# Optimization experiments

Measured on AMD Instinct MI355X. Metric: run time of the kernel, lower is better.

The kernel has to match this reference:

```python
import jax, jax.numpy as jnp
import numpy as np

B, N, DEG = 256, 16384, 32  # batch, num_neurons, fan-in per neuron

def setup_inputs() -> dict:
    key = jax.random.key(0)
    kx, kw, ki = jax.random.split(key, 3)
    x = jax.random.normal(kx, (B, N), dtype=jnp.float32)
    w = jax.random.normal(kw, (N, DEG), dtype=jnp.float32)  # nonzero weights per neuron
    idx = jax.random.randint(ki, (N, DEG), 0, N)            # source-neuron indices per neuron
    return {"x": x, "w": w, "idx": idx}

def reference(x, w, idx):
    # Per neuron j: gather its fan-in channels and apply Dense(1) with
    # kernel = nonzero weights, then relu; concat over neurons == axis N.
    gathered = x[:, idx]                      # [B, N, DEG] gather
    out = jnp.einsum('bnd,nd->bn', gathered, w)  # sparse matvec per batch row
    return jax.nn.relu(out)                   # [B, N]
```

## Files before the change

### kernel.cpp

```cpp
#include <hip/hip_runtime.h>


#define NB   16384
#define DEG  32

typedef __fp16 hp2 __attribute__((ext_vector_type(2)));

__device__ __forceinline__ unsigned pk16(float a, float b) {
    return __builtin_bit_cast(unsigned, (hp2)__builtin_amdgcn_cvt_pkrtz(a, b));
}

__global__ __launch_bounds__(256) void prep_pw_kernel(
    const int* __restrict__ idx, const float* __restrict__ w,
    uint4* __restrict__ pw4) {
    __shared__ int   idx_s[64][33];
    __shared__ float w_s[64][33];
    const int t  = threadIdx.x;
    const int nb = (int)blockIdx.x * 64;

    const int4*   src  = (const int4*)(idx + (size_t)nb * DEG);
    const float4* srcw = (const float4*)(w   + (size_t)nb * DEG);
#pragma unroll
    for (int p = 0; p < 2; ++p) {
        const int e4 = t + 256 * p;
        const int n0 = e4 >> 3;
        const int c0 = (e4 & 7) * 4;
        const int4 v = src[e4];
        idx_s[n0][c0 + 0] = v.x; idx_s[n0][c0 + 1] = v.y;
        idx_s[n0][c0 + 2] = v.z; idx_s[n0][c0 + 3] = v.w;
        const float4 f = srcw[e4];
        w_s[n0][c0 + 0] = f.x; w_s[n0][c0 + 1] = f.y;
        w_s[n0][c0 + 2] = f.z; w_s[n0][c0 + 3] = f.w;
    }
    __syncthreads();

    const int np    = t & 63;
    const int dbase = t >> 6;
#pragma unroll
    for (int k = 0; k < 2; ++k) {
        const int d4 = dbase * 2 + k;
        const int c  = 4 * d4;
        uint4 o;
        o.x = (unsigned)idx_s[np][c + 0] | ((unsigned)idx_s[np][c + 1] << 16);
        o.y = pk16(w_s[np][c + 0], w_s[np][c + 1]);
        o.z = (unsigned)idx_s[np][c + 2] | ((unsigned)idx_s[np][c + 3] << 16);
        o.w = pk16(w_s[np][c + 2], w_s[np][c + 3]);
        pw4[(size_t)d4 * NB + nb + np] = o;
    }
}

#define LOADQ(buf, nn)                                                     \
    do {                                                                   \
        const uint4* p_ = pw4 + (nn);                                      \
        _Pragma("unroll") for (int d4_ = 0; d4_ < 8; ++d4_)                \
            buf[d4_] = p_[(size_t)d4_ * NB];                               \
    } while (0)

#define GISSUE(K)                                                          \
    {                                                                      \
        const unsigned jA_ = Q[K].x;                                       \
        g[K][0] = lds[jA_ & 0xffffu];                                      \
        g[K][1] = lds[jA_ >> 16];                                          \
        const unsigned jB_ = Q[K].z;                                       \
        g[K][2] = lds[jB_ & 0xffffu];                                      \
        g[K][3] = lds[jB_ >> 16];                                          \
    }

#define GFMA(K, r01, r23)                                                  \
    {                                                                      \
        const hp2 wA_  = __builtin_bit_cast(hp2, Q[K].y);                  \
        const hp2 wAlo = {wA_.x, wA_.x};                                   \
        const hp2 wAhi = {wA_.y, wA_.y};                                   \
        r01 += wAlo * __builtin_bit_cast(hp2, g[K][0].x);                  \
        r23 += wAlo * __builtin_bit_cast(hp2, g[K][0].y);                  \
        r01 += wAhi * __builtin_bit_cast(hp2, g[K][1].x);                  \
        r23 += wAhi * __builtin_bit_cast(hp2, g[K][1].y);                  \
        const hp2 wB_  = __builtin_bit_cast(hp2, Q[K].w);                  \
        const hp2 wBlo = {wB_.x, wB_.x};                                   \
        const hp2 wBhi = {wB_.y, wB_.y};                                   \
        r01 += wBlo * __builtin_bit_cast(hp2, g[K][2].x);                  \
        r23 += wBlo * __builtin_bit_cast(hp2, g[K][2].y);                  \
        r01 += wBhi * __builtin_bit_cast(hp2, g[K][3].x);                  \
        r23 += wBhi * __builtin_bit_cast(hp2, g[K][3].y);                  \
    }

#define STEP(I, LD)                                                        \
    {                                                                      \
        const int n = n0 + t + 1024 * (I);                                 \
        if (LD) LOADQ(Q, n);                                               \
        uint2 g[8][4];                                                     \
        GISSUE(0) GISSUE(1) GISSUE(2) GISSUE(3)                            \
        hp2 a01 = {0, 0}, a23 = {0, 0}, c01 = {0, 0}, c23 = {0, 0};        \
        GFMA(0, a01, a23) GISSUE(4)                                        \
        GFMA(1, a01, a23) GISSUE(5)                                        \
        GFMA(2, a01, a23) GISSUE(6)                                        \
        GFMA(3, a01, a23) GISSUE(7)                                        \
        GFMA(4, c01, c23)                                                  \
        GFMA(5, c01, c23)                                                  \
        GFMA(6, c01, c23)                                                  \
        GFMA(7, c01, c23)                                                  \
        const hp2 s01 = a01 + c01;                                         \
        const hp2 s23 = a23 + c23;                                         \
        __builtin_nontemporal_store(fmaxf((float)s01.x, 0.f),              \
                                    &out[(size_t)(b0 + 0) * NB + n]);      \
        __builtin_nontemporal_store(fmaxf((float)s01.y, 0.f),              \
                                    &out[(size_t)(b0 + 1) * NB + n]);      \
        __builtin_nontemporal_store(fmaxf((float)s23.x, 0.f),              \
                                    &out[(size_t)(b0 + 2) * NB + n]);      \
        __builtin_nontemporal_store(fmaxf((float)s23.y, 0.f),              \
                                    &out[(size_t)(b0 + 3) * NB + n]);      \
    }

__global__ __launch_bounds__(1024, 4) void gather4_kernel(
    const float* __restrict__ x, const uint4* __restrict__ pw4,
    float* __restrict__ out) {
    extern __shared__ uint2 lds[];
    const int t  = threadIdx.x;
    const int q  = (int)blockIdx.x & 63;
    const int n0 = ((int)blockIdx.x >> 6) * 4096;

    const float* xr0 = x + (size_t)(4 * q) * NB;
    const float* xr1 = xr0 + NB;
    const float* xr2 = xr1 + NB;
    const float* xr3 = xr2 + NB;
#pragma unroll
    for (int p = 0; p < 4; ++p) {
        const int j = 4 * (t + 1024 * p);
        const float4 r0 = *(const float4*)&xr0[j];
        const float4 r1 = *(const float4*)&xr1[j];
        const float4 r2 = *(const float4*)&xr2[j];
        const float4 r3 = *(const float4*)&xr3[j];
        uint4 w0, w1;
        w0.x = pk16(r0.x, r1.x); w0.y = pk16(r2.x, r3.x);
        w0.z = pk16(r0.y, r1.y); w0.w = pk16(r2.y, r3.y);
        w1.x = pk16(r0.z, r1.z); w1.y = pk16(r2.z, r3.z);
        w1.z = pk16(r0.w, r1.w); w1.w = pk16(r2.w, r3.w);
        *(uint4*)&lds[j]     = w0;
        *(uint4*)&lds[j + 2] = w1;
    }

    uint4 Q[8];
    LOADQ(Q, n0 + t);
    __syncthreads();

    const int b0 = 4 * q;
    STEP(0, 0)
    STEP(1, 1)
    STEP(2, 1)
    STEP(3, 1)
}

extern "C" void kernel_launch(void* const* d_in, const int* in_sizes, int n_in,
                              void* d_out, int out_size, void* d_ws, size_t ws_size,
                              hipStream_t stream) {
    const float* x   = (const float*)d_in[0];
    const float* w   = (const float*)d_in[1];
    const int*   idx = (const int*)d_in[2];
    float* out = (float*)d_out;
    uint4* pw4 = (uint4*)d_ws;

    (void)hipFuncSetAttribute((const void*)gather4_kernel,
                              hipFuncAttributeMaxDynamicSharedMemorySize, 131072);

    prep_pw_kernel<<<NB / 64, 256, 0, stream>>>(idx, w, pw4);

    gather4_kernel<<<256, 1024, 131072, stream>>>(x, pw4, out);
}
```

Before: 83.83 us.

## Process two batch rows per block instead of four to halve LDS footprint

```diff
diff --git a/kernel.cpp b/kernel.cpp
--- a/kernel.cpp
+++ b/kernel.cpp
@@ -59,91 +59,77 @@
 #define GISSUE(K)                                                          \
     {                                                                      \
         const unsigned jA_ = Q[K].x;                                       \
-        g[K][0] = lds[jA_ & 0xffffu];                                      \
-        g[K][1] = lds[jA_ >> 16];                                          \
+        g[K][0] = lds32[jA_ & 0xffffu];                                    \
+        g[K][1] = lds32[jA_ >> 16];                                        \
         const unsigned jB_ = Q[K].z;                                       \
-        g[K][2] = lds[jB_ & 0xffffu];                                      \
-        g[K][3] = lds[jB_ >> 16];                                          \
+        g[K][2] = lds32[jB_ & 0xffffu];                                    \
+        g[K][3] = lds32[jB_ >> 16];                                        \
     }
 
-#define GFMA(K, r01, r23)                                                  \
+#define GFMA(K, r01)                                                       \
     {                                                                      \
         const hp2 wA_  = __builtin_bit_cast(hp2, Q[K].y);                  \
         const hp2 wAlo = {wA_.x, wA_.x};                                   \
         const hp2 wAhi = {wA_.y, wA_.y};                                   \
-        r01 += wAlo * __builtin_bit_cast(hp2, g[K][0].x);                  \
-        r23 += wAlo * __builtin_bit_cast(hp2, g[K][0].y);                  \
-        r01 += wAhi * __builtin_bit_cast(hp2, g[K][1].x);                  \
-        r23 += wAhi * __builtin_bit_cast(hp2, g[K][1].y);                  \
+        r01 += wAlo * __builtin_bit_cast(hp2, g[K][0]);                    \
+        r01 += wAhi * __builtin_bit_cast(hp2, g[K][1]);                    \
         const hp2 wB_  = __builtin_bit_cast(hp2, Q[K].w);                  \
         const hp2 wBlo = {wB_.x, wB_.x};                                   \
         const hp2 wBhi = {wB_.y, wB_.y};                                   \
-        r01 += wBlo * __builtin_bit_cast(hp2, g[K][2].x);                  \
-        r23 += wBlo * __builtin_bit_cast(hp2, g[K][2].y);                  \
-        r01 += wBhi * __builtin_bit_cast(hp2, g[K][3].x);                  \
-        r23 += wBhi * __builtin_bit_cast(hp2, g[K][3].y);                  \
+        r01 += wBlo * __builtin_bit_cast(hp2, g[K][2]);                    \
+        r01 += wBhi * __builtin_bit_cast(hp2, g[K][3]);                    \
     }
 
 #define STEP(I, LD)                                                        \
     {                                                                      \
         const int n = n0 + t + 1024 * (I);                                 \
         if (LD) LOADQ(Q, n);                                               \
-        uint2 g[8][4];                                                     \
+        unsigned g[8][4];                                                  \
         GISSUE(0) GISSUE(1) GISSUE(2) GISSUE(3)                            \
-        hp2 a01 = {0, 0}, a23 = {0, 0}, c01 = {0, 0}, c23 = {0, 0};        \
-        GFMA(0, a01, a23) GISSUE(4)                                        \
-        GFMA(1, a01, a23) GISSUE(5)                                        \
-        GFMA(2, a01, a23) GISSUE(6)                                        \
-        GFMA(3, a01, a23) GISSUE(7)                                        \
-        GFMA(4, c01, c23)                                                  \
-        GFMA(5, c01, c23)                                                  \
-        GFMA(6, c01, c23)                                                  \
-        GFMA(7, c01, c23)                                                  \
+        hp2 a01 = {0, 0}, c01 = {0, 0};                                    \
+        GFMA(0, a01) GISSUE(4)                                             \
+        GFMA(1, a01) GISSUE(5)                                             \
+        GFMA(2, a01) GISSUE(6)                                             \
+        GFMA(3, a01) GISSUE(7)                                             \
+        GFMA(4, c01)                                                       \
+        GFMA(5, c01)                                                       \
+        GFMA(6, c01)                                                       \
+        GFMA(7, c01)                                                       \
         const hp2 s01 = a01 + c01;                                         \
-        const hp2 s23 = a23 + c23;                                         \
         __builtin_nontemporal_store(fmaxf((float)s01.x, 0.f),              \
                                     &out[(size_t)(b0 + 0) * NB + n]);      \
         __builtin_nontemporal_store(fmaxf((float)s01.y, 0.f),              \
                                     &out[(size_t)(b0 + 1) * NB + n]);      \
-        __builtin_nontemporal_store(fmaxf((float)s23.x, 0.f),              \
-                                    &out[(size_t)(b0 + 2) * NB + n]);      \
-        __builtin_nontemporal_store(fmaxf((float)s23.y, 0.f),              \
-                                    &out[(size_t)(b0 + 3) * NB + n]);      \
     }
 
-__global__ __launch_bounds__(1024, 4) void gather4_kernel(
+__global__ __launch_bounds__(1024, 8) void gather2_kernel(
     const float* __restrict__ x, const uint4* __restrict__ pw4,
     float* __restrict__ out) {
-    extern __shared__ uint2 lds[];
+    extern __shared__ unsigned lds32[];
     const int t  = threadIdx.x;
-    const int q  = (int)blockIdx.x & 63;
-    const int n0 = ((int)blockIdx.x >> 6) * 4096;
+    const int pr = (int)blockIdx.x & 127;
+    const int n0 = ((int)blockIdx.x >> 7) * 4096;
 
-    const float* xr0 = x + (size_t)(4 * q) * NB;
+    const float* xr0 = x + (size_t)(2 * pr) * NB;
     const float* xr1 = xr0 + NB;
-    const float* xr2 = xr1 + NB;
-    const float* xr3 = xr2 + NB;
 #pragma unroll
     for (int p = 0; p < 4; ++p) {
         const int j = 4 * (t + 1024 * p);
         const float4 r0 = *(const float4*)&xr0[j];
         const float4 r1 = *(const float4*)&xr1[j];
-        const float4 r2 = *(const float4*)&xr2[j];
-        const float4 r3 = *(const float4*)&xr3[j];
-        uint4 w0, w1;
-        w0.x = pk16(r0.x, r1.x); w0.y = pk16(r2.x, r3.x);
-        w0.z = pk16(r0.y, r1.y); w0.w = pk16(r2.y, r3.y);
-        w1.x = pk16(r0.z, r1.z); w1.y = pk16(r2.z, r3.z);
-        w1.z = pk16(r0.w, r1.w); w1.w = pk16(r2.w, r3.w);
-        *(uint4*)&lds[j]     = w0;
-        *(uint4*)&lds[j + 2] = w1;
+        uint4 w0;
+        w0.x = pk16(r0.x, r1.x);
+        w0.y = pk16(r0.y, r1.y);
+        w0.z = pk16(r0.z, r1.z);
+        w0.w = pk16(r0.w, r1.w);
+        *(uint4*)&lds32[j] = w0;
     }
 
     uint4 Q[8];
     LOADQ(Q, n0 + t);
     __syncthreads();
 
-    const int b0 = 4 * q;
+    const int b0 = 2 * pr;
     STEP(0, 0)
     STEP(1, 1)
     STEP(2, 1)
@@ -159,10 +145,10 @@
     float* out = (float*)d_out;
     uint4* pw4 = (uint4*)d_ws;
 
-    (void)hipFuncSetAttribute((const void*)gather4_kernel,
-                              hipFuncAttributeMaxDynamicSharedMemorySize, 131072);
+    (void)hipFuncSetAttribute((const void*)gather2_kernel,
+                              hipFuncAttributeMaxDynamicSharedMemorySize, 65536);
 
     prep_pw_kernel<<<NB / 64, 256, 0, stream>>>(idx, w, pw4);
 
-    gather4_kernel<<<256, 1024, 131072, stream>>>(x, pw4, out);
+    gather2_kernel<<<512, 1024, 65536, stream>>>(x, pw4, out);
 }
```

Measured after the change: 89.24 us. 1.06x slower.

## Drop prep kernel and read raw idx and weights inside gather kernel

Applied to the files above, without the earlier changes.

```diff
diff --git a/kernel.cpp b/kernel.cpp
--- a/kernel.cpp
+++ b/kernel.cpp
@@ -10,95 +10,45 @@
     return __builtin_bit_cast(unsigned, (hp2)__builtin_amdgcn_cvt_pkrtz(a, b));
 }
 
-__global__ __launch_bounds__(256) void prep_pw_kernel(
-    const int* __restrict__ idx, const float* __restrict__ w,
-    uint4* __restrict__ pw4) {
-    __shared__ int   idx_s[64][33];
-    __shared__ float w_s[64][33];
-    const int t  = threadIdx.x;
-    const int nb = (int)blockIdx.x * 64;
-
-    const int4*   src  = (const int4*)(idx + (size_t)nb * DEG);
-    const float4* srcw = (const float4*)(w   + (size_t)nb * DEG);
-#pragma unroll
-    for (int p = 0; p < 2; ++p) {
-        const int e4 = t + 256 * p;
-        const int n0 = e4 >> 3;
-        const int c0 = (e4 & 7) * 4;
-        const int4 v = src[e4];
-        idx_s[n0][c0 + 0] = v.x; idx_s[n0][c0 + 1] = v.y;
-        idx_s[n0][c0 + 2] = v.z; idx_s[n0][c0 + 3] = v.w;
-        const float4 f = srcw[e4];
-        w_s[n0][c0 + 0] = f.x; w_s[n0][c0 + 1] = f.y;
-        w_s[n0][c0 + 2] = f.z; w_s[n0][c0 + 3] = f.w;
-    }
-    __syncthreads();
-
-    const int np    = t & 63;
-    const int dbase = t >> 6;
-#pragma unroll
-    for (int k = 0; k < 2; ++k) {
-        const int d4 = dbase * 2 + k;
-        const int c  = 4 * d4;
-        uint4 o;
-        o.x = (unsigned)idx_s[np][c + 0] | ((unsigned)idx_s[np][c + 1] << 16);
-        o.y = pk16(w_s[np][c + 0], w_s[np][c + 1]);
-        o.z = (unsigned)idx_s[np][c + 2] | ((unsigned)idx_s[np][c + 3] << 16);
-        o.w = pk16(w_s[np][c + 2], w_s[np][c + 3]);
-        pw4[(size_t)d4 * NB + nb + np] = o;
-    }
-}
-
-#define LOADQ(buf, nn)                                                     \
+#define LOADIW(nn)                                                         \
     do {                                                                   \
-        const uint4* p_ = pw4 + (nn);                                      \
-        _Pragma("unroll") for (int d4_ = 0; d4_ < 8; ++d4_)                \
-            buf[d4_] = p_[(size_t)d4_ * NB];                               \
+        const int4*   ip_ = (const int4*)(idx + (size_t)(nn) * DEG);       \
+        const float4* wp_ = (const float4*)(w   + (size_t)(nn) * DEG);     \
+        _Pragma("unroll") for (int k_ = 0; k_ < 8; ++k_) {                 \
+            I[k_] = ip_[k_];                                               \
+            W[k_] = wp_[k_];                                               \
+        }                                                                  \
     } while (0)
 
-#define GISSUE(K)                                                          \
+#define PAIR(jA, jB, wA, wB, r01, r23)                                     \
     {                                                                      \
-        const unsigned jA_ = Q[K].x;                                       \
-        g[K][0] = lds[jA_ & 0xffffu];                                      \
-        g[K][1] = lds[jA_ >> 16];                                          \
-        const unsigned jB_ = Q[K].z;                                       \
-        g[K][2] = lds[jB_ & 0xffffu];                                      \
-        g[K][3] = lds[jB_ >> 16];                                          \
+        const uint2 g0_ = lds[(unsigned)(jA)];                             \
+        const uint2 g1_ = lds[(unsigned)(jB)];                             \
+        const hp2 wlo_ = (hp2)__builtin_amdgcn_cvt_pkrtz(wA, wA);          \
+        const hp2 whi_ = (hp2)__builtin_amdgcn_cvt_pkrtz(wB, wB);          \
+        r01 += wlo_ * __builtin_bit_cast(hp2, g0_.x);                      \
+        r23 += wlo_ * __builtin_bit_cast(hp2, g0_.y);                      \
+        r01 += whi_ * __builtin_bit_cast(hp2, g1_.x);                      \
+        r23 += whi_ * __builtin_bit_cast(hp2, g1_.y);                      \
     }
 
-#define GFMA(K, r01, r23)                                                  \
+#define QUAD(K, r01, r23)                                                  \
+    PAIR(I[K].x, I[K].y, W[K].x, W[K].y, r01, r23)                         \
+    PAIR(I[K].z, I[K].w, W[K].z, W[K].w, r01, r23)
+
+#define STEP(II, LD)                                                       \
     {                                                                      \
-        const hp2 wA_  = __builtin_bit_cast(hp2, Q[K].y);                  \
-        const hp2 wAlo = {wA_.x, wA_.x};                                   \
-        const hp2 wAhi = {wA_.y, wA_.y};                                   \
-        r01 += wAlo * __builtin_bit_cast(hp2, g[K][0].x);                  \
-        r23 += wAlo * __builtin_bit_cast(hp2, g[K][0].y);                  \
-        r01 += wAhi * __builtin_bit_cast(hp2, g[K][1].x);                  \
-        r23 += wAhi * __builtin_bit_cast(hp2, g[K][1].y);                  \
-        const hp2 wB_  = __builtin_bit_cast(hp2, Q[K].w);                  \
-        const hp2 wBlo = {wB_.x, wB_.x};                                   \
-        const hp2 wBhi = {wB_.y, wB_.y};                                   \
-        r01 += wBlo * __builtin_bit_cast(hp2, g[K][2].x);                  \
-        r23 += wBlo * __builtin_bit_cast(hp2, g[K][2].y);                  \
-        r01 += wBhi * __builtin_bit_cast(hp2, g[K][3].x);                  \
-        r23 += wBhi * __builtin_bit_cast(hp2, g[K][3].y);                  \
-    }
-
-#define STEP(I, LD)                                                        \
-    {                                                                      \
-        const int n = n0 + t + 1024 * (I);                                 \
-        if (LD) LOADQ(Q, n);                                               \
-        uint2 g[8][4];                                                     \
-        GISSUE(0) GISSUE(1) GISSUE(2) GISSUE(3)                            \
+        const int n = n0 + t + 1024 * (II);                                \
+        if (LD) LOADIW(n);                                                 \
         hp2 a01 = {0, 0}, a23 = {0, 0}, c01 = {0, 0}, c23 = {0, 0};        \
-        GFMA(0, a01, a23) GISSUE(4)                                        \
-        GFMA(1, a01, a23) GISSUE(5)                                        \
-        GFMA(2, a01, a23) GISSUE(6)                                        \
-        GFMA(3, a01, a23) GISSUE(7)                                        \
-        GFMA(4, c01, c23)                                                  \
-        GFMA(5, c01, c23)                                                  \
-        GFMA(6, c01, c23)                                                  \
-        GFMA(7, c01, c23)                                                  \
+        QUAD(0, a01, a23)                                                  \
+        QUAD(1, a01, a23)                                                  \
+        QUAD(2, a01, a23)                                                  \
+        QUAD(3, a01, a23)                                                  \
+        QUAD(4, c01, c23)                                                  \
+        QUAD(5, c01, c23)                                                  \
+        QUAD(6, c01, c23)                                                  \
+        QUAD(7, c01, c23)                                                  \
         const hp2 s01 = a01 + c01;                                         \
         const hp2 s23 = a23 + c23;                                         \
         __builtin_nontemporal_store(fmaxf((float)s01.x, 0.f),              \
@@ -112,8 +62,8 @@
     }
 
 __global__ __launch_bounds__(1024, 4) void gather4_kernel(
-    const float* __restrict__ x, const uint4* __restrict__ pw4,
-    float* __restrict__ out) {
+    const float* __restrict__ x, const int* __restrict__ idx,
+    const float* __restrict__ w, float* __restrict__ out) {
     extern __shared__ uint2 lds[];
     const int t  = threadIdx.x;
     const int q  = (int)blockIdx.x & 63;
@@ -139,8 +89,9 @@
         *(uint4*)&lds[j + 2] = w1;
     }
 
-    uint4 Q[8];
-    LOADQ(Q, n0 + t);
+    int4   I[8];
+    float4 W[8];
+    LOADIW(n0 + t);
     __syncthreads();
 
     const int b0 = 4 * q;
@@ -157,12 +108,10 @@
     const float* w   = (const float*)d_in[1];
     const int*   idx = (const int*)d_in[2];
     float* out = (float*)d_out;
-    uint4* pw4 = (uint4*)d_ws;
+    (void)d_ws; (void)ws_size;
 
     (void)hipFuncSetAttribute((const void*)gather4_kernel,
                               hipFuncAttributeMaxDynamicSharedMemorySize, 131072);
 
-    prep_pw_kernel<<<NB / 64, 256, 0, stream>>>(idx, w, pw4);
-
-    gather4_kernel<<<256, 1024, 131072, stream>>>(x, pw4, out);
+    gather4_kernel<<<256, 1024, 131072, stream>>>(x, idx, w, out);
 }
```

Result: slower. 117.3 us (+39.9%).
